# Performance work log

Hardware: AMD Instinct MI355X
Metric: run time of the kernel (lower is better)

The kernel has to match this reference:

```python
import jax, jax.numpy as jnp
import numpy as np

N_NODES = 10000
D_IN = 128
D_OUT = 128
N_EDGES = 640000


def setup_inputs() -> dict:
    key = jax.random.key(0)
    k_x, k_e, k_wl, k_wr, k_b = jax.random.split(key, 5)
    x = jax.random.normal(k_x, (N_NODES, D_IN), dtype=jnp.float32)
    edge_index = jax.random.randint(k_e, (2, N_EDGES), 0, N_NODES, dtype=jnp.int64)
    # SAGEConv params: lin_l (neighbor path, with bias), lin_r (root path, no bias)
    s_l = 1.0 / np.sqrt(D_IN)
    W_l = jax.random.uniform(k_wl, (D_OUT, D_IN), dtype=jnp.float32, minval=-s_l, maxval=s_l)
    b_l = jax.random.uniform(k_b, (D_OUT,), dtype=jnp.float32, minval=-s_l, maxval=s_l)
    W_r = jax.random.uniform(k_wr, (D_OUT, D_IN), dtype=jnp.float32, minval=-s_l, maxval=s_l)
    return {"x": x, "edge_index": edge_index, "W_l": W_l, "b_l": b_l, "W_r": W_r}


def reference(x, edge_index, W_l, b_l, W_r):
    x = x.astype(jnp.float32)
    src, dst = edge_index[0], edge_index[1]
    # gather source features, mean-aggregate into destination nodes
    msgs = x[src]                                   # [E, D_in] irregular gather
    agg_sum = jax.ops.segment_sum(msgs, dst, num_segments=N_NODES)  # [N, D_in]
    deg = jax.ops.segment_sum(jnp.ones((src.shape[0],), dtype=x.dtype), dst,
                              num_segments=N_NODES)                 # [N]
    agg = jnp.where(deg[:, None] > 0, agg_sum / jnp.maximum(deg, 1.0)[:, None], 0.0)
    # SAGEConv: lin_l(agg) + lin_r(x)
    y = agg @ W_l.T + b_l + x @ W_r.T               # [N, D_out]
    return x + y                                     # residual add
```

## Files before the change

### kernel.cpp

```cpp
#include <hip/hip_runtime.h>

#define N_NODES 10000
#define D 128
#define N_EDGES 640000
#define NB 128
#define EPB (N_EDGES / NB)
#define SB 40
#define NPSB 250


__global__ __launch_bounds__(1024) void hist_local_kernel(const int* __restrict__ ei,
                                                          unsigned short* __restrict__ lrank,
                                                          unsigned short* __restrict__ cnt,
                                                          unsigned long long* __restrict__ flags) {
    __shared__ int h[N_NODES];
    for (int n = threadIdx.x; n < N_NODES; n += 1024) h[n] = 0;
    if (blockIdx.x == 0 && threadIdx.x < SB) flags[threadIdx.x] = 0ULL;
    __syncthreads();
    const int base = blockIdx.x * EPB;
    for (int e = base + threadIdx.x; e < base + EPB; e += 1024) {
        int d = ei[N_EDGES + e];
        lrank[e] = (unsigned short)atomicAdd(&h[d], 1);
    }
    __syncthreads();
    unsigned short* c = cnt + (size_t)blockIdx.x * N_NODES;
    for (int n = threadIdx.x; n < N_NODES; n += 1024) c[n] = (unsigned short)h[n];
}

__global__ __launch_bounds__(256) void colscan_scan_kernel(unsigned short* __restrict__ cnt,
                                                           int* __restrict__ row_start,
                                                           unsigned long long* __restrict__ flags) {
    const int t = threadIdx.x;
    const int b = blockIdx.x;
    const int n = b * NPSB + t;
    __shared__ int sc[256];
    __shared__ int blk_excl_sh;

    int deg = 0;
    if (t < NPSB) {
        int s = 0;
#pragma unroll 8
        for (int j = 0; j < NB; ++j) {
            int idx = j * N_NODES + n;
            int v = cnt[idx];
            cnt[idx] = (unsigned short)s;
            s += v;
        }
        deg = s;
    }
    sc[t] = deg;
    __syncthreads();
    for (int off = 1; off < 256; off <<= 1) {
        int v = (t >= off) ? sc[t - off] : 0;
        __syncthreads();
        sc[t] += v;
        __syncthreads();
    }
    const int total = sc[255];
    const int local_excl = sc[t] - deg;

    if (t == 0) {
        int excl = 0;
        if (b == 0) {
            __hip_atomic_store(&flags[0], (2ULL << 32) | (unsigned)total,
                               __ATOMIC_RELEASE, __HIP_MEMORY_SCOPE_AGENT);
        } else {
            __hip_atomic_store(&flags[b], (1ULL << 32) | (unsigned)total,
                               __ATOMIC_RELEASE, __HIP_MEMORY_SCOPE_AGENT);
            int j = b - 1;
            while (j >= 0) {
                unsigned long long f = __hip_atomic_load(&flags[j], __ATOMIC_ACQUIRE,
                                                         __HIP_MEMORY_SCOPE_AGENT);
                unsigned st = (unsigned)(f >> 32);
                if (st == 0) continue;
                excl += (int)(unsigned)(f & 0xffffffffULL);
                if (st == 2) break;
                --j;
            }
            __hip_atomic_store(&flags[b], (2ULL << 32) | (unsigned)(excl + total),
                               __ATOMIC_RELEASE, __HIP_MEMORY_SCOPE_AGENT);
        }
        blk_excl_sh = excl;
    }
    __syncthreads();
    if (t < NPSB) row_start[n] = blk_excl_sh + local_excl;
    if (b == SB - 1 && t == 0) row_start[N_NODES] = N_EDGES;
}

__global__ __launch_bounds__(256) void scatter_kernel(const int* __restrict__ ei,
                                                      const int* __restrict__ row_start,
                                                      const unsigned short* __restrict__ cnt,
                                                      const unsigned short* __restrict__ lrank,
                                                      int* __restrict__ csr) {
    int i = blockIdx.x * 256 + threadIdx.x;
    if (i < N_EDGES) {
        int b = i / EPB;
        int s = ei[i];
        int d = ei[N_EDGES + i];
        int pos = row_start[d] + (int)cnt[b * N_NODES + d] + (int)lrank[i];
        csr[pos] = s;
    }
}


__device__ __forceinline__ void f4add(float4& a, const float4& v) {
    a.x += v.x; a.y += v.y; a.z += v.z; a.w += v.w;
}

__global__ __launch_bounds__(128) void aggregate_kernel(const float4* __restrict__ x4,
                                                        const int* __restrict__ row_start,
                                                        const int* __restrict__ csr,
                                                        float4* __restrict__ agg4) {
    __shared__ int idx[256];
    __shared__ float4 red[4][32];
    const int node = blockIdx.x;
    const int lane = threadIdx.x & 31;
    const int slot = threadIdx.x >> 5;
    const int start = row_start[node];
    const int end = row_start[node + 1];

    float4 a0 = {0,0,0,0}, a1 = {0,0,0,0}, a2 = {0,0,0,0}, a3 = {0,0,0,0};
    for (int cs = start; cs < end; cs += 256) {
        int m = min(256, end - cs);
        if ((int)threadIdx.x < m) idx[threadIdx.x] = csr[cs + threadIdx.x];
        if ((int)threadIdx.x + 128 < m) idx[threadIdx.x + 128] = csr[cs + threadIdx.x + 128];
        __syncthreads();
        int j = slot;
        for (; j + 12 < m; j += 16) {
            int s0 = idx[j], s1 = idx[j + 4], s2 = idx[j + 8], s3 = idx[j + 12];
            float4 v0 = x4[s0 * 32 + lane];
            float4 v1 = x4[s1 * 32 + lane];
            float4 v2 = x4[s2 * 32 + lane];
            float4 v3 = x4[s3 * 32 + lane];
            f4add(a0, v0); f4add(a1, v1); f4add(a2, v2); f4add(a3, v3);
        }
        for (; j < m; j += 4) {
            float4 v = x4[idx[j] * 32 + lane];
            f4add(a0, v);
        }
        __syncthreads();
    }
    f4add(a0, a1); f4add(a2, a3); f4add(a0, a2);
    red[slot][lane] = a0;
    __syncthreads();
    if (slot == 0) {
        float4 a = red[0][lane], b = red[1][lane], c = red[2][lane], d = red[3][lane];
        int cntE = end - start;
        float inv = (cntE > 0) ? 1.0f / (float)cntE : 0.0f;
        float4 o;
        o.x = ((a.x + b.x) + (c.x + d.x)) * inv;
        o.y = ((a.y + b.y) + (c.y + d.y)) * inv;
        o.z = ((a.z + b.z) + (c.z + d.z)) * inv;
        o.w = ((a.w + b.w) + (c.w + d.w)) * inv;
        agg4[node * 32 + lane] = o;
    }
}


__global__ __launch_bounds__(128) void lin_kernel(const float* __restrict__ x,
                                                  const float* __restrict__ agg,
                                                  const float* __restrict__ Wl,
                                                  const float* __restrict__ bl,
                                                  const float* __restrict__ Wr,
                                                  float* __restrict__ out) {
    __shared__ float4 xs[8][32];
    __shared__ float4 as[8][32];
    float* xsf = (float*)xs;
    float* asf = (float*)as;
    const int f = threadIdx.x;
    const int n0 = blockIdx.x * 8;

    for (int n = 0; n < 8; ++n) {
        xsf[n * D + f] = x[(n0 + n) * D + f];
        asf[n * D + f] = agg[(n0 + n) * D + f];
    }
    __syncthreads();

    float bias = bl[f];
    float acc[8];
#pragma unroll
    for (int n = 0; n < 8; ++n) acc[n] = bias;

    const float4* wl4 = (const float4*)(Wl + f * D);
    const float4* wr4 = (const float4*)(Wr + f * D);
    for (int kk = 0; kk < 32; ++kk) {
        float4 wl = wl4[kk];
        float4 wr = wr4[kk];
#pragma unroll
        for (int n = 0; n < 8; ++n) {
            float4 a = as[n][kk];
            float4 xv = xs[n][kk];
            acc[n] += a.x * wl.x + a.y * wl.y + a.z * wl.z + a.w * wl.w;
            acc[n] += xv.x * wr.x + xv.y * wr.y + xv.z * wr.z + xv.w * wr.w;
        }
    }

    for (int n = 0; n < 8; ++n) {
        out[(n0 + n) * D + f] = xsf[n * D + f] + acc[n];
    }
}

extern "C" void kernel_launch(void* const* d_in, const int* in_sizes, int n_in,
                              void* d_out, int out_size, void* d_ws, size_t ws_size,
                              hipStream_t stream) {
    const float* x  = (const float*)d_in[0];
    const int*   ei = (const int*)d_in[1];
    const float* Wl = (const float*)d_in[2];
    const float* bl = (const float*)d_in[3];
    const float* Wr = (const float*)d_in[4];
    float* out = (float*)d_out;

    unsigned long long* flags = (unsigned long long*)d_ws;
    int* row_start = (int*)(flags + 64);
    unsigned short* cnt   = (unsigned short*)(row_start + 10016);
    unsigned short* lrank = cnt + (size_t)NB * N_NODES;
    int* csr   = (int*)(lrank + N_EDGES);
    float* agg = (float*)(csr + N_EDGES);

    hist_local_kernel<<<NB, 1024, 0, stream>>>(ei, lrank, cnt, flags);
    colscan_scan_kernel<<<SB, 256, 0, stream>>>(cnt, row_start, flags);
    scatter_kernel<<<(N_EDGES + 255) / 256, 256, 0, stream>>>(ei, row_start, cnt, lrank, csr);
    aggregate_kernel<<<N_NODES, 128, 0, stream>>>((const float4*)x, row_start, csr,
                                                  (float4*)agg);
    lin_kernel<<<N_NODES / 8, 128, 0, stream>>>(x, agg, Wl, bl, Wr, out);
}
```

Baseline: 144.1 us.

## Gather bf16 copies of node features and store CSR indices as 16-bit

A new kernel first casts x to bf16, and the aggregation then gathers these 8-byte rows instead of 16-byte fp32 rows. This halves the bytes moved by the random-access gather. CSR source indices are also stored as 16-bit values, which fits because there are fewer than 65536 nodes, and the linear kernel now handles 16 nodes per block instead of 8. The cost is an extra cast pass, plus a loss of precision in the aggregated mean from rounding inputs to bf16.

```diff
diff --git a/kernel.cpp b/kernel.cpp
--- a/kernel.cpp
+++ b/kernel.cpp
@@ -7,6 +7,29 @@
 #define EPB (N_EDGES / NB)
 #define SB 40
 #define NPSB 250
+
+
+__device__ __forceinline__ unsigned short f2bf(float f) {
+    union { float f; unsigned int i; } v;
+    v.f = f;
+    unsigned int b = v.i;
+    unsigned int rounded = b + 0x7fffu + ((b >> 16) & 1u);
+    return (unsigned short)(rounded >> 16);
+}
+
+__global__ __launch_bounds__(256) void cast_kernel(const float4* __restrict__ x4,
+                                                   ushort4* __restrict__ xh4) {
+    int i = blockIdx.x * 256 + threadIdx.x;
+    if (i < N_NODES * D / 4) {
+        float4 v = x4[i];
+        ushort4 o;
+        o.x = f2bf(v.x);
+        o.y = f2bf(v.y);
+        o.z = f2bf(v.z);
+        o.w = f2bf(v.w);
+        xh4[i] = o;
+    }
+}
 
 
 __global__ __launch_bounds__(1024) void hist_local_kernel(const int* __restrict__ ei,
@@ -91,27 +114,33 @@
                                                       const int* __restrict__ row_start,
                                                       const unsigned short* __restrict__ cnt,
                                                       const unsigned short* __restrict__ lrank,
-                                                      int* __restrict__ csr) {
+                                                      unsigned short* __restrict__ csr) {
     int i = blockIdx.x * 256 + threadIdx.x;
     if (i < N_EDGES) {
         int b = i / EPB;
         int s = ei[i];
         int d = ei[N_EDGES + i];
         int pos = row_start[d] + (int)cnt[b * N_NODES + d] + (int)lrank[i];
-        csr[pos] = s;
-    }
-}
-
-
-__device__ __forceinline__ void f4add(float4& a, const float4& v) {
-    a.x += v.x; a.y += v.y; a.z += v.z; a.w += v.w;
-}
-
-__global__ __launch_bounds__(128) void aggregate_kernel(const float4* __restrict__ x4,
+        csr[pos] = (unsigned short)s;
+    }
+}
+
+
+__device__ __forceinline__ float bf2f(unsigned short u) {
+    union { unsigned int i; float f; } v;
+    v.i = ((unsigned int)u) << 16;
+    return v.f;
+}
+
+__device__ __forceinline__ void bf4add(float4& a, const ushort4& v) {
+    a.x += bf2f(v.x); a.y += bf2f(v.y); a.z += bf2f(v.z); a.w += bf2f(v.w);
+}
+
+__global__ __launch_bounds__(128) void aggregate_kernel(const ushort4* __restrict__ xh4,
                                                         const int* __restrict__ row_start,
-                                                        const int* __restrict__ csr,
+                                                        const unsigned short* __restrict__ csr,
                                                         float4* __restrict__ agg4) {
-    __shared__ int idx[256];
+    __shared__ unsigned short idxs[256];
     __shared__ float4 red[4][32];
     const int node = blockIdx.x;
     const int lane = threadIdx.x & 31;
@@ -122,25 +151,27 @@
     float4 a0 = {0,0,0,0}, a1 = {0,0,0,0}, a2 = {0,0,0,0}, a3 = {0,0,0,0};
     for (int cs = start; cs < end; cs += 256) {
         int m = min(256, end - cs);
-        if ((int)threadIdx.x < m) idx[threadIdx.x] = csr[cs + threadIdx.x];
-        if ((int)threadIdx.x + 128 < m) idx[threadIdx.x + 128] = csr[cs + threadIdx.x + 128];
+        if ((int)threadIdx.x < m) idxs[threadIdx.x] = csr[cs + threadIdx.x];
+        if ((int)threadIdx.x + 128 < m) idxs[threadIdx.x + 128] = csr[cs + threadIdx.x + 128];
         __syncthreads();
         int j = slot;
         for (; j + 12 < m; j += 16) {
-            int s0 = idx[j], s1 = idx[j + 4], s2 = idx[j + 8], s3 = idx[j + 12];
-            float4 v0 = x4[s0 * 32 + lane];
-            float4 v1 = x4[s1 * 32 + lane];
-            float4 v2 = x4[s2 * 32 + lane];
-            float4 v3 = x4[s3 * 32 + lane];
-            f4add(a0, v0); f4add(a1, v1); f4add(a2, v2); f4add(a3, v3);
+            int s0 = idxs[j], s1 = idxs[j + 4], s2 = idxs[j + 8], s3 = idxs[j + 12];
+            ushort4 v0 = xh4[s0 * 32 + lane];
+            ushort4 v1 = xh4[s1 * 32 + lane];
+            ushort4 v2 = xh4[s2 * 32 + lane];
+            ushort4 v3 = xh4[s3 * 32 + lane];
+            bf4add(a0, v0); bf4add(a1, v1); bf4add(a2, v2); bf4add(a3, v3);
         }
         for (; j < m; j += 4) {
-            float4 v = x4[idx[j] * 32 + lane];
-            f4add(a0, v);
-        }
-        __syncthreads();
-    }
-    f4add(a0, a1); f4add(a2, a3); f4add(a0, a2);
+            ushort4 v = xh4[(int)idxs[j] * 32 + lane];
+            bf4add(a0, v);
+        }
+        __syncthreads();
+    }
+    a0.x += a1.x; a0.y += a1.y; a0.z += a1.z; a0.w += a1.w;
+    a2.x += a3.x; a2.y += a3.y; a2.z += a3.z; a2.w += a3.w;
+    a0.x += a2.x; a0.y += a2.y; a0.z += a2.z; a0.w += a2.w;
     red[slot][lane] = a0;
     __syncthreads();
     if (slot == 0) {
@@ -163,40 +194,48 @@
                                                   const float* __restrict__ bl,
                                                   const float* __restrict__ Wr,
                                                   float* __restrict__ out) {
-    __shared__ float4 xs[8][32];
-    __shared__ float4 as[8][32];
-    float* xsf = (float*)xs;
-    float* asf = (float*)as;
+    __shared__ float xs[16 * D];
+    __shared__ float as[16 * D];
     const int f = threadIdx.x;
-    const int n0 = blockIdx.x * 8;
-
-    for (int n = 0; n < 8; ++n) {
-        xsf[n * D + f] = x[(n0 + n) * D + f];
-        asf[n * D + f] = agg[(n0 + n) * D + f];
+    const int n0 = blockIdx.x * 16;
+
+    {
+        const float4* xsrc = (const float4*)(x + n0 * D);
+        const float4* asrc = (const float4*)(agg + n0 * D);
+        float4* xd = (float4*)xs;
+        float4* ad = (float4*)as;
+#pragma unroll
+        for (int c = 0; c < 4; ++c) {
+            xd[c * 128 + f] = xsrc[c * 128 + f];
+            ad[c * 128 + f] = asrc[c * 128 + f];
+        }
     }
     __syncthreads();
 
     float bias = bl[f];
-    float acc[8];
-#pragma unroll
-    for (int n = 0; n < 8; ++n) acc[n] = bias;
+    float acc[16];
+#pragma unroll
+    for (int n = 0; n < 16; ++n) acc[n] = bias;
 
     const float4* wl4 = (const float4*)(Wl + f * D);
     const float4* wr4 = (const float4*)(Wr + f * D);
+    const float4* as4 = (const float4*)as;
+    const float4* xs4 = (const float4*)xs;
     for (int kk = 0; kk < 32; ++kk) {
         float4 wl = wl4[kk];
         float4 wr = wr4[kk];
 #pragma unroll
-        for (int n = 0; n < 8; ++n) {
-            float4 a = as[n][kk];
-            float4 xv = xs[n][kk];
+        for (int n = 0; n < 16; ++n) {
+            float4 a = as4[n * 32 + kk];
+            float4 xv = xs4[n * 32 + kk];
             acc[n] += a.x * wl.x + a.y * wl.y + a.z * wl.z + a.w * wl.w;
             acc[n] += xv.x * wr.x + xv.y * wr.y + xv.z * wr.z + xv.w * wr.w;
         }
     }
 
-    for (int n = 0; n < 8; ++n) {
-        out[(n0 + n) * D + f] = xsf[n * D + f] + acc[n];
+#pragma unroll
+    for (int n = 0; n < 16; ++n) {
+        out[(n0 + n) * D + f] = xs[n * D + f] + acc[n];
     }
 }
 
@@ -214,13 +253,16 @@
     int* row_start = (int*)(flags + 64);
     unsigned short* cnt   = (unsigned short*)(row_start + 10016);
     unsigned short* lrank = cnt + (size_t)NB * N_NODES;
-    int* csr   = (int*)(lrank + N_EDGES);
-    float* agg = (float*)(csr + N_EDGES);
-
+    unsigned short* csr   = lrank + N_EDGES;
+    unsigned short* xh    = csr + N_EDGES;
+    float* agg = (float*)(xh + (size_t)N_NODES * D);
+
+    cast_kernel<<<(N_NODES * D / 4 + 255) / 256, 256, 0, stream>>>(
+        (const float4*)x, (ushort4*)xh);
     hist_local_kernel<<<NB, 1024, 0, stream>>>(ei, lrank, cnt, flags);
     colscan_scan_kernel<<<SB, 256, 0, stream>>>(cnt, row_start, flags);
     scatter_kernel<<<(N_EDGES + 255) / 256, 256, 0, stream>>>(ei, row_start, cnt, lrank, csr);
-    aggregate_kernel<<<N_NODES, 128, 0, stream>>>((const float4*)x, row_start, csr,
+    aggregate_kernel<<<N_NODES, 128, 0, stream>>>((const ushort4*)xh, row_start, csr,
                                                   (float4*)agg);
-    lin_kernel<<<N_NODES / 8, 128, 0, stream>>>(x, agg, Wl, bl, Wr, out);
-}
+    lin_kernel<<<N_NODES / 16, 128, 0, stream>>>(x, agg, Wl, bl, Wr, out);
+}
```

Result: slower. 153.5 us (+6.5%).
